# Kernel tuning notes

Measured on AMD Instinct MI355X. Metric: run time of the kernel, lower is better.

## Reference

```python
import jax, jax.numpy as jnp
import numpy as np

NUM_GROUPS = 8
NUM_HEADS = 4
EPS = 1e-5


def group_norm(x, w, b):
    # x: [B, C, H, W]; normalize over (C/G, H, W) within each of G groups
    B, C, H, W = x.shape
    xg = x.reshape(B, NUM_GROUPS, C // NUM_GROUPS, H, W)
    mean = xg.mean(axis=(2, 3, 4), keepdims=True)
    var = xg.var(axis=(2, 3, 4), keepdims=True)
    xn = ((xg - mean) * jax.lax.rsqrt(var + EPS)).reshape(B, C, H, W)
    return xn * w[None, :, None, None] + b[None, :, None, None]


def setup_inputs() -> dict:
    key = jax.random.key(0)
    ks = jax.random.split(key, 7)
    B, C, H, W = 4, 256, 64, 64
    x = jax.random.normal(ks[0], (B, C, H, W), dtype=jnp.float32)
    gn_w = jax.random.normal(ks[1], (C,), dtype=jnp.float32) * 0.1 + 1.0
    gn_b = jax.random.normal(ks[2], (C,), dtype=jnp.float32) * 0.1
    qkv_w = jax.random.normal(ks[3], (3 * C, C), dtype=jnp.float32) / np.sqrt(C)
    qkv_b = jax.random.normal(ks[4], (3 * C,), dtype=jnp.float32) * 0.02
    proj_w = jax.random.normal(ks[5], (C, C), dtype=jnp.float32) / np.sqrt(C)
    proj_b = jax.random.normal(ks[6], (C,), dtype=jnp.float32) * 0.02
    return {"x": x, "gn_w": gn_w, "gn_b": gn_b, "qkv_w": qkv_w,
            "qkv_b": qkv_b, "proj_w": proj_w, "proj_b": proj_b}


def reference(x, gn_w, gn_b, qkv_w, qkv_b, proj_w, proj_b):
    B, C, H, W = x.shape
    nh = NUM_HEADS
    hd = C // nh
    scale = hd ** -0.5
    N = H * W

    h = group_norm(x, gn_w, gn_b)
    # 1x1 conv == channel matmul: [B, 3C, H, W]
    qkv = jnp.einsum('oc,bchw->bohw', qkv_w, h) + qkv_b[None, :, None, None]
    qkv = qkv.reshape(B, 3, nh, hd, N)  # matches torch .view(B,3,nh,hd,HW)
    q, k, v = qkv[:, 0], qkv[:, 1], qkv[:, 2]  # each [B, nh, hd, N]

    attn = jnp.einsum('bhdn,bhdm->bhnm', q, k) * scale  # [B, nh, N, N]
    attn = jax.nn.softmax(attn, axis=-1)
    out = jnp.einsum('bhnm,bhdm->bhdn', attn, v)  # [B, nh, hd, N]
    out = out.reshape(B, C, H, W)

    proj = jnp.einsum('oc,bchw->bohw', proj_w, out) + proj_b[None, :, None, None]
    return x + proj
```

## Files before the change

kernel.cpp:

```cpp
#include <hip/hip_runtime.h>
#include <hip/hip_bf16.h>

#define BB   4
#define CC   256
#define NN   4096
#define NH   4
#define HD   64
#define NG   8
#define GSZ  32
#define EPSV 1e-5f
#define SCALE_L2E 0.18033688f

typedef __bf16 bf16x8 __attribute__((ext_vector_type(8)));
typedef float  f32x4  __attribute__((ext_vector_type(4)));

#define MFMA16(a, b, c)  __builtin_amdgcn_mfma_f32_16x16x32_bf16((a), (b), (c), 0, 0, 0)

#if __has_builtin(__builtin_amdgcn_exp2f)
#define EXP2F __builtin_amdgcn_exp2f
#else
#define EXP2F exp2f
#endif

__device__ inline unsigned short f2bf(float f) {
    unsigned int u = __float_as_uint(f);
    u += 0x7fffu + ((u >> 16) & 1u);
    return (unsigned short)(u >> 16);
}

__device__ __forceinline__ bf16x8 pk8(const f32x4& p0, const f32x4& p1) {
    alignas(16) unsigned int u[4];
    u[0] = __builtin_amdgcn_perm(__float_as_uint(p0[1]), __float_as_uint(p0[0]), 0x07060302u);
    u[1] = __builtin_amdgcn_perm(__float_as_uint(p0[3]), __float_as_uint(p0[2]), 0x07060302u);
    u[2] = __builtin_amdgcn_perm(__float_as_uint(p1[1]), __float_as_uint(p1[0]), 0x07060302u);
    u[3] = __builtin_amdgcn_perm(__float_as_uint(p1[3]), __float_as_uint(p1[2]), 0x07060302u);
    return *reinterpret_cast<bf16x8*>(u);
}

__device__ __forceinline__ void async_ld16(void* lds, const void* g) {
    __builtin_amdgcn_global_load_lds(
        (const __attribute__((address_space(1))) unsigned int*)g,
        (__attribute__((address_space(3))) unsigned int*)lds, 16, 0, 0);
}

__global__ void k_prep(const float* __restrict__ x, float* __restrict__ stats,
                       const float* __restrict__ wq, const float* __restrict__ wp,
                       unsigned short* __restrict__ oq, unsigned short* __restrict__ op) {
    int blk = blockIdx.x;
    int t = threadIdx.x;
    if (blk >= 256) {
        int i = (blk - 256) * 256 + t;
        if (i < 3 * CC * CC) oq[i] = f2bf(wq[i]);
        if (i < CC * CC)     op[i] = f2bf(wp[i]);
        return;
    }
    int b = blk >> 6, g = (blk >> 3) & 7, s = blk & 7;
    const float* p = x + ((size_t)(b * CC + g * GSZ)) * NN + s * 16384;
    float s0 = 0.f, s1 = 0.f;
    #pragma unroll
    for (int i = 0; i < 64; ++i) { float v = p[i * 256 + t]; s0 += v; s1 += v * v; }
    #pragma unroll
    for (int m = 1; m <= 32; m <<= 1) { s0 += __shfl_xor(s0, m); s1 += __shfl_xor(s1, m); }
    __shared__ float ls[8];
    int w = t >> 6;
    if ((t & 63) == 0) { ls[w * 2] = s0; ls[w * 2 + 1] = s1; }
    __syncthreads();
    if (t == 0) {
        float a0 = ls[0] + ls[2] + ls[4] + ls[6];
        float a1 = ls[1] + ls[3] + ls[5] + ls[7];
        atomicAdd(&stats[(b * NG + g) * 2 + 0], a0);
        atomicAdd(&stats[(b * NG + g) * 2 + 1], a1);
    }
}

__global__ void k_gnapply(const float* __restrict__ x, const float* __restrict__ gw,
                          const float* __restrict__ gb, const float* __restrict__ stats,
                          unsigned short* __restrict__ ht) {
    int b = blockIdx.z, ct = blockIdx.y, nt = blockIdx.x;
    int c0 = ct * 32, n0 = nt * 64;
    int t = threadIdx.x;
    __shared__ float tile[32][65];
    const float* xp = x + ((size_t)(b * CC + c0)) * NN + n0;
    int cl = t >> 6, nl = t & 63;
    #pragma unroll
    for (int p = 0; p < 8; ++p)
        tile[p * 4 + cl][nl] = xp[(size_t)(p * 4 + cl) * NN + nl];
    float sum = stats[(b * NG + ct) * 2 + 0];
    float ssq = stats[(b * NG + ct) * 2 + 1];
    float mean = sum * (1.0f / 131072.0f);
    float var  = ssq * (1.0f / 131072.0f) - mean * mean;
    float inv  = rsqrtf(var + EPSV);
    __syncthreads();
    int nw = t >> 2, ci = (t & 3) * 8;
    alignas(16) unsigned short o8[8];
    #pragma unroll
    for (int j = 0; j < 8; ++j) {
        int c = c0 + ci + j;
        float v = (tile[ci + j][nw] - mean) * inv * gw[c] + gb[c];
        o8[j] = f2bf(v);
    }
    *reinterpret_cast<uint4*>(ht + ((size_t)(b * NN + n0 + nw)) * CC + c0 + ci) =
        *reinterpret_cast<const uint4*>(o8);
}

__global__ void __launch_bounds__(256)
k_qkv(const unsigned short* __restrict__ ht, const unsigned short* __restrict__ wq,
      const float* __restrict__ qb,
      unsigned short* __restrict__ qt, unsigned short* __restrict__ kt,
      unsigned short* __restrict__ vt) {
    int bx = blockIdx.x, by = blockIdx.y;
    int t = threadIdx.x, wave = t >> 6, lane = t & 63;
    int l15 = lane & 15, quad = lane >> 4;
    int wm = wave >> 1, wn = wave & 1;

    __shared__ alignas(16) unsigned char smem[33792];

    const char* Ag = (const char*)wq + (size_t)by * 65536;
    const char* Bg = (const char*)ht + (size_t)bx * 65536;
    int row0 = t >> 2, slot = t & 3;
    size_t a0 = (size_t)row0 * 512 + slot * 16;
    size_t a1 = a0 + 64 * 512;
    unsigned int dst0 = wave * 1024;

    auto stage = [&](int buf, int kk) {
        size_t ko = (size_t)kk * 64;
        unsigned char* Ab = smem + buf * 8192;
        unsigned char* Bb = smem + 16384 + buf * 8192;
        async_ld16(Ab + dst0,        Ag + a0 + ko);
        async_ld16(Ab + 4096 + dst0, Ag + a1 + ko);
        async_ld16(Bb + dst0,        Bg + a0 + ko);
        async_ld16(Bb + 4096 + dst0, Bg + a1 + ko);
    };

    f32x4 acc[4][4];
    #pragma unroll
    for (int i = 0; i < 4; ++i)
        #pragma unroll
        for (int j = 0; j < 4; ++j) acc[i][j] = (f32x4){0.f, 0.f, 0.f, 0.f};

    stage(0, 0);
    __syncthreads();

    for (int kk = 0; kk < 8; ++kk) {
        int cur = kk & 1;
        if (kk < 7) stage(cur ^ 1, kk + 1);
        bf16x8 af[4], bf[4];
        #pragma unroll
        for (int f = 0; f < 4; ++f) {
            af[f] = *reinterpret_cast<const bf16x8*>(smem + cur * 8192 + (wm * 64 + f * 16 + l15) * 64 + quad * 16);
            bf[f] = *reinterpret_cast<const bf16x8*>(smem + 16384 + cur * 8192 + (wn * 64 + f * 16 + l15) * 64 + quad * 16);
        }
        #pragma unroll
        for (int fm = 0; fm < 4; ++fm)
            #pragma unroll
            for (int fn = 0; fn < 4; ++fn)
                acc[fm][fn] = MFMA16(af[fm], bf[fn], acc[fm][fn]);
        __syncthreads();
    }

    int s = by >> 1;
    int nn0 = bx * 128;
    int b = nn0 >> 12, nbase = nn0 & 4095;
    if (s < 2) {
        #pragma unroll
        for (int fm = 0; fm < 4; ++fm) {
            int o = by * 128 + wm * 64 + fm * 16 + quad * 4;
            int h = (o >> 6) & 3, d0 = o & 63;
            float bias[4];
            #pragma unroll
            for (int r = 0; r < 4; ++r) bias[r] = qb[o + r];
            #pragma unroll
            for (int fn = 0; fn < 4; ++fn) {
                int n = nbase + wn * 64 + fn * 16 + l15;
                alignas(8) unsigned short o4[4];
                if (s == 0) {
                    #pragma unroll
                    for (int r = 0; r < 4; ++r) o4[r] = f2bf((acc[fm][fn][r] + bias[r]) * SCALE_L2E);
                    *reinterpret_cast<uint2*>(qt + (((size_t)(b * NH + h) * NN) + n) * HD + d0) =
                        *reinterpret_cast<const uint2*>(o4);
                } else {
                    #pragma unroll
                    for (int r = 0; r < 4; ++r) o4[r] = f2bf(acc[fm][fn][r] + bias[r]);
                    *reinterpret_cast<uint2*>(kt + (((size_t)(b * NH + h) * NN) + n) * HD + d0) =
                        *reinterpret_cast<const uint2*>(o4);
                }
            }
        }
    } else {
        unsigned short* vtile = (unsigned short*)smem;
        #pragma unroll
        for (int fm = 0; fm < 4; ++fm) {
            int o  = by * 128 + wm * 64 + fm * 16 + quad * 4;
            int ol = wm * 64 + fm * 16 + quad * 4;
            float bias[4];
            #pragma unroll
            for (int r = 0; r < 4; ++r) bias[r] = qb[o + r];
            #pragma unroll
            for (int fn = 0; fn < 4; ++fn) {
                int nl = wn * 64 + fn * 16 + l15;
                #pragma unroll
                for (int r = 0; r < 4; ++r)
                    vtile[(ol + r) * 132 + nl] = f2bf(acc[fm][fn][r] + bias[r]);
            }
        }
        __syncthreads();
        int hbase = (by - 4) * 2;
        #pragma unroll
        for (int pass = 0; pass < 8; ++pass) {
            int row  = pass * 16 + (t >> 4);
            int col0 = (t & 15) * 8;
            int nb = (col0 & ~31) | ((col0 & 16) >> 1) | ((col0 & 8) >> 1);
            const unsigned short* src = vtile + row * 132 + nb;
            uint2 lo = *reinterpret_cast<const uint2*>(src);
            uint2 hi = *reinterpret_cast<const uint2*>(src + 16);
            uint4 o4 = make_uint4(lo.x, lo.y, hi.x, hi.y);
            int h = hbase + (row >> 6), d = row & 63;
            *reinterpret_cast<uint4*>(vt + ((size_t)(b * NH + h) * HD + d) * NN + nbase + col0) = o4;
        }
    }
}

__global__ void __launch_bounds__(256, 4)
k_attn(const unsigned short* __restrict__ qt, const unsigned short* __restrict__ kt,
       const unsigned short* __restrict__ vt,
       unsigned short* __restrict__ op0, unsigned short* __restrict__ op1,
       float* __restrict__ lip) {
    int bh = blockIdx.y;
    int split = blockIdx.z;
    int t = threadIdx.x, wave = t >> 6, lane = t & 63;
    int l15 = lane & 15, quad = lane >> 4;
    int qbase = blockIdx.x * 128 + wave * 32;
    int kbase = split * 2048;
    const unsigned short* qp = qt + (size_t)bh * NN * HD;
    const unsigned short* kp = kt + (size_t)bh * NN * HD;
    const unsigned short* vp = vt + (size_t)bh * HD * NN;

    __shared__ alignas(16) unsigned char kbuf[2][8192];
    __shared__ alignas(16) unsigned char vbuf[2][8192];

    int lr8 = lane >> 3, lc8 = lane & 7;
    int swz = lc8 ^ lr8;
    const char* ksrc = (const char*)kp + (size_t)(kbase + wave * 16 + lr8) * 128 + swz * 16;
    const char* vsrc = (const char*)vp + (size_t)(wave * 16 + lr8) * 8192 + (size_t)kbase * 2 + swz * 16;
    unsigned int dstw = wave * 2048;

    auto stage = [&](int buf) {
        async_ld16(kbuf[buf] + dstw,        ksrc);
        async_ld16(kbuf[buf] + dstw + 1024, ksrc + 1024);
        ksrc += 8192;
        async_ld16(vbuf[buf] + dstw,        vsrc);
        async_ld16(vbuf[buf] + dstw + 1024, vsrc + 8 * 8192);
        vsrc += 128;
    };

    bf16x8 qaA0 = *reinterpret_cast<const bf16x8*>(qp + (size_t)(qbase + l15) * HD + quad * 8);
    bf16x8 qaA1 = *reinterpret_cast<const bf16x8*>(qp + (size_t)(qbase + l15) * HD + 32 + quad * 8);
    bf16x8 qaB0 = *reinterpret_cast<const bf16x8*>(qp + (size_t)(qbase + 16 + l15) * HD + quad * 8);
    bf16x8 qaB1 = *reinterpret_cast<const bf16x8*>(qp + (size_t)(qbase + 16 + l15) * HD + 32 + quad * 8);

    const f32x4 Z4 = (f32x4){0.f, 0.f, 0.f, 0.f};
    bf16x8 vone;
    #pragma unroll
    for (int i = 0; i < 8; ++i) vone[i] = (__bf16)1.0f;

    f32x4 OA[4], OB[4];
    #pragma unroll
    for (int i = 0; i < 4; ++i) { OA[i] = Z4; OB[i] = Z4; }
    f32x4 liAA = Z4, liBB = Z4;

    int sx = l15 & 7;

    auto compute = [&](const unsigned char* kb, const unsigned char* vbb) {
        f32x4 sA0[2], sA1[2], sB0[2], sB1[2];
        #pragma unroll
        for (int s = 0; s < 2; ++s) {
            int r0 = (s * 32 + l15) * 128;
            bf16x8 k00 = *reinterpret_cast<const bf16x8*>(kb + r0 + ((quad ^ sx) * 16));
            bf16x8 k01 = *reinterpret_cast<const bf16x8*>(kb + r0 + (((quad + 4) ^ sx) * 16));
            bf16x8 k10 = *reinterpret_cast<const bf16x8*>(kb + r0 + 2048 + ((quad ^ sx) * 16));
            bf16x8 k11 = *reinterpret_cast<const bf16x8*>(kb + r0 + 2048 + (((quad + 4) ^ sx) * 16));
            sA0[s] = MFMA16(k00, qaA0, Z4);  sA0[s] = MFMA16(k01, qaA1, sA0[s]);
            sA1[s] = MFMA16(k10, qaA0, Z4);  sA1[s] = MFMA16(k11, qaA1, sA1[s]);
            sB0[s] = MFMA16(k00, qaB0, Z4);  sB0[s] = MFMA16(k01, qaB1, sB0[s]);
            sB1[s] = MFMA16(k10, qaB0, Z4);  sB1[s] = MFMA16(k11, qaB1, sB1[s]);
        }
        #pragma unroll
        for (int s = 0; s < 2; ++s) {
            f32x4 pA0, pA1, pB0, pB1;
            #pragma unroll
            for (int r = 0; r < 4; ++r) {
                pA0[r] = EXP2F(sA0[s][r]);  pA1[r] = EXP2F(sA1[s][r]);
                pB0[r] = EXP2F(sB0[s][r]);  pB1[r] = EXP2F(sB1[s][r]);
            }
            bf16x8 fA = pk8(pA0, pA1);
            bf16x8 fB = pk8(pB0, pB1);

            liAA = MFMA16(fA, vone, liAA);
            liBB = MFMA16(fB, vone, liBB);

            #pragma unroll
            for (int dc = 0; dc < 4; ++dc) {
                const unsigned char* vrow = vbb + (dc * 16 + l15) * 128;
                bf16x8 vv = *reinterpret_cast<const bf16x8*>(vrow + (((s * 4 + quad) ^ sx) * 16));
                OA[dc] = MFMA16(fA, vv, OA[dc]);
                OB[dc] = MFMA16(fB, vv, OB[dc]);
            }
        }
    };

    stage(0);
    __syncthreads();

    for (int p = 0; p < 16; ++p) {
        stage(1);
        compute(kbuf[0], vbuf[0]);
        __syncthreads();
        if (p < 15) stage(0);
        compute(kbuf[1], vbuf[1]);
        __syncthreads();
    }

    unsigned short* op = split ? op1 : op0;
    int b = bh >> 2, h = bh & 3;
    #pragma unroll
    for (int dc = 0; dc < 4; ++dc) {
        #pragma unroll
        for (int r = 0; r < 4; ++r) {
            int qA = qbase + quad * 4 + r;
            op[((size_t)(b * NN) + qA) * CC + h * HD + dc * 16 + l15]      = f2bf(OA[dc][r]);
            op[((size_t)(b * NN) + qA + 16) * CC + h * HD + dc * 16 + l15] = f2bf(OB[dc][r]);
        }
    }
    float* lp = lip + (size_t)split * (16 * NN) + (size_t)bh * NN + qbase;
    if (l15 == 0) {
        #pragma unroll
        for (int r = 0; r < 4; ++r) {
            lp[quad * 4 + r]      = liAA[r];
            lp[16 + quad * 4 + r] = liBB[r];
        }
    }
}

__global__ void __launch_bounds__(256)
k_comb(unsigned short* ao, const unsigned short* __restrict__ p1, const float* __restrict__ lip) {
    int g = blockIdx.x * 256 + threadIdx.x;
    int d8 = g & 7;
    int h  = (g >> 3) & 3;
    int n  = (g >> 5) & 4095;
    int b  = g >> 17;
    int bh = b * 4 + h;
    float li0 = lip[(size_t)bh * NN + n];
    float li1 = lip[(size_t)16 * NN + (size_t)bh * NN + n];
    float inv = 1.0f / (li0 + li1);
    size_t idx = ((size_t)(b * NN) + n) * CC + h * HD + d8 * 8;
    uint4 u0 = *reinterpret_cast<const uint4*>(ao + idx);
    uint4 u1 = *reinterpret_cast<const uint4*>(p1 + idx);
    const unsigned short* a0 = reinterpret_cast<const unsigned short*>(&u0);
    const unsigned short* a1 = reinterpret_cast<const unsigned short*>(&u1);
    alignas(16) unsigned short o8[8];
    #pragma unroll
    for (int i = 0; i < 8; ++i) {
        float f0 = __uint_as_float((unsigned)a0[i] << 16);
        float f1 = __uint_as_float((unsigned)a1[i] << 16);
        o8[i] = f2bf((f0 + f1) * inv);
    }
    *reinterpret_cast<uint4*>(ao + idx) = *reinterpret_cast<const uint4*>(o8);
}

__global__ void __launch_bounds__(256)
k_proj(const unsigned short* __restrict__ ao, const unsigned short* __restrict__ wp,
       const float* __restrict__ pb, const float* __restrict__ x,
       float* __restrict__ out) {
    int bx = blockIdx.x, by = blockIdx.y;
    int t = threadIdx.x, wave = t >> 6, lane = t & 63;
    int l15 = lane & 15, quad = lane >> 4;
    int wm = wave >> 1, wn = wave & 1;

    __shared__ alignas(16) unsigned char At[2][4096];
    __shared__ alignas(16) unsigned char Bt[2][4096];

    const char* Ag = (const char*)wp + (size_t)by * 32768;
    const char* Bg = (const char*)ao + (size_t)bx * 32768;
    int row0 = t >> 2, slot = t & 3;
    size_t a0 = (size_t)row0 * 512 + slot * 16;
    unsigned int dst0 = wave * 1024;

    auto stage = [&](int buf, int kk) {
        size_t ko = (size_t)kk * 64;
        async_ld16(At[buf] + dst0, Ag + a0 + ko);
        async_ld16(Bt[buf] + dst0, Bg + a0 + ko);
    };

    f32x4 acc[2][2];
    #pragma unroll
    for (int i = 0; i < 2; ++i)
        #pragma unroll
        for (int j = 0; j < 2; ++j) acc[i][j] = (f32x4){0.f, 0.f, 0.f, 0.f};

    stage(0, 0);
    __syncthreads();

    for (int kk = 0; kk < 8; ++kk) {
        int cur = kk & 1;
        if (kk < 7) stage(cur ^ 1, kk + 1);
        bf16x8 af[2], bf[2];
        #pragma unroll
        for (int f = 0; f < 2; ++f) {
            af[f] = *reinterpret_cast<const bf16x8*>(At[cur] + (wm * 32 + f * 16 + l15) * 64 + quad * 16);
            bf[f] = *reinterpret_cast<const bf16x8*>(Bt[cur] + (wn * 32 + f * 16 + l15) * 64 + quad * 16);
        }
        #pragma unroll
        for (int fm = 0; fm < 2; ++fm)
            #pragma unroll
            for (int fn = 0; fn < 2; ++fn)
                acc[fm][fn] = MFMA16(af[fm], bf[fn], acc[fm][fn]);
        __syncthreads();
    }

    int nn0 = bx * 64;
    int b = nn0 >> 12, nbase = nn0 & 4095;
    #pragma unroll
    for (int fm = 0; fm < 2; ++fm) {
        int o = by * 64 + wm * 32 + fm * 16 + quad * 4;
        float bias[4];
        #pragma unroll
        for (int r = 0; r < 4; ++r) bias[r] = pb[o + r];
        #pragma unroll
        for (int fn = 0; fn < 2; ++fn) {
            int n = nbase + wn * 32 + fn * 16 + l15;
            #pragma unroll
            for (int r = 0; r < 4; ++r) {
                size_t idx = ((size_t)(b * CC + o + r)) * NN + n;
                out[idx] = acc[fm][fn][r] + bias[r] + x[idx];
            }
        }
    }
}

extern "C" void kernel_launch(void* const* d_in, const int* in_sizes, int n_in,
                              void* d_out, int out_size, void* d_ws, size_t ws_size,
                              hipStream_t stream) {
    const float* x     = (const float*)d_in[0];
    const float* gw    = (const float*)d_in[1];
    const float* gb    = (const float*)d_in[2];
    const float* qkvw  = (const float*)d_in[3];
    const float* qkvb  = (const float*)d_in[4];
    const float* projw = (const float*)d_in[5];
    const float* projb = (const float*)d_in[6];
    float* out = (float*)d_out;

    char* w = (char*)d_ws;
    size_t off = 0;
    unsigned short* ht = (unsigned short*)(w + off); off += (size_t)BB * NN * CC * 2;
    unsigned short* qt = (unsigned short*)(w + off); off += (size_t)BB * NH * NN * HD * 2;
    unsigned short* kt = (unsigned short*)(w + off); off += (size_t)BB * NH * NN * HD * 2;
    unsigned short* vt = (unsigned short*)(w + off); off += (size_t)BB * NH * HD * NN * 2;
    unsigned short* ao = (unsigned short*)(w + off); off += (size_t)BB * NN * CC * 2;
    unsigned short* wqb = (unsigned short*)(w + off); off += (size_t)3 * CC * CC * 2;
    unsigned short* wpb = (unsigned short*)(w + off); off += (size_t)CC * CC * 2;
    float* stats = (float*)(w + off); off += BB * NG * 2 * sizeof(float);
    float* lip   = (float*)(w + off); off += (size_t)2 * 16 * NN * sizeof(float);

    hipMemsetAsync(stats, 0, BB * NG * 2 * sizeof(float), stream);
    k_prep<<<1024, 256, 0, stream>>>(x, stats, qkvw, projw, wqb, wpb);
    k_gnapply<<<dim3(NN / 64, CC / 32, BB), 256, 0, stream>>>(x, gw, gb, stats, ht);
    k_qkv<<<dim3(BB * NN / 128, 6), 256, 0, stream>>>(ht, wqb, qkvb, qt, kt, vt);
    k_attn<<<dim3(NN / 128, BB * NH, 2), 256, 0, stream>>>(qt, kt, vt, ao, ht, lip);
    k_comb<<<2048, 256, 0, stream>>>(ao, ht, lip);
    k_proj<<<dim3(BB * NN / 64, CC / 64), 256, 0, stream>>>(ao, wpb, projb, x, out);
}
```

Measured before the change: 188.7 us.

## Split attention keys four ways and raise wave priority around MFMA blocks

Splits the key dimension of the attention kernel into four chunks instead of two. This doubles the grid (32x16x4 blocks) so more CUs are busy, and each block runs half as many iterations. The partial outputs and row sums go to extra workspace buffers and are merged in the combine kernel. It also wraps the MFMA sections in s_setprio so matrix work from different waves interleaves with the exp work. The cost is more partial-output traffic to write and read back in the combine step, plus a larger workspace.

```diff
diff --git a/kernel.cpp b/kernel.cpp
--- a/kernel.cpp
+++ b/kernel.cpp
@@ -224,13 +224,14 @@
 k_attn(const unsigned short* __restrict__ qt, const unsigned short* __restrict__ kt,
        const unsigned short* __restrict__ vt,
        unsigned short* __restrict__ op0, unsigned short* __restrict__ op1,
+       unsigned short* __restrict__ op2, unsigned short* __restrict__ op3,
        float* __restrict__ lip) {
     int bh = blockIdx.y;
     int split = blockIdx.z;
     int t = threadIdx.x, wave = t >> 6, lane = t & 63;
     int l15 = lane & 15, quad = lane >> 4;
     int qbase = blockIdx.x * 128 + wave * 32;
-    int kbase = split * 2048;
+    int kbase = split * 1024;
     const unsigned short* qp = qt + (size_t)bh * NN * HD;
     const unsigned short* kp = kt + (size_t)bh * NN * HD;
     const unsigned short* vp = vt + (size_t)bh * HD * NN;
@@ -272,6 +273,7 @@
 
     auto compute = [&](const unsigned char* kb, const unsigned char* vbb) {
         f32x4 sA0[2], sA1[2], sB0[2], sB1[2];
+        __builtin_amdgcn_s_setprio(1);
         #pragma unroll
         for (int s = 0; s < 2; ++s) {
             int r0 = (s * 32 + l15) * 128;
@@ -284,6 +286,7 @@
             sB0[s] = MFMA16(k00, qaB0, Z4);  sB0[s] = MFMA16(k01, qaB1, sB0[s]);
             sB1[s] = MFMA16(k10, qaB0, Z4);  sB1[s] = MFMA16(k11, qaB1, sB1[s]);
         }
+        __builtin_amdgcn_s_setprio(0);
         #pragma unroll
         for (int s = 0; s < 2; ++s) {
             f32x4 pA0, pA1, pB0, pB1;
@@ -295,6 +298,7 @@
             bf16x8 fA = pk8(pA0, pA1);
             bf16x8 fB = pk8(pB0, pB1);
 
+            __builtin_amdgcn_s_setprio(1);
             liAA = MFMA16(fA, vone, liAA);
             liBB = MFMA16(fB, vone, liBB);
 
@@ -305,22 +309,23 @@
                 OA[dc] = MFMA16(fA, vv, OA[dc]);
                 OB[dc] = MFMA16(fB, vv, OB[dc]);
             }
+            __builtin_amdgcn_s_setprio(0);
         }
     };
 
     stage(0);
     __syncthreads();
 
-    for (int p = 0; p < 16; ++p) {
+    for (int p = 0; p < 8; ++p) {
         stage(1);
         compute(kbuf[0], vbuf[0]);
         __syncthreads();
-        if (p < 15) stage(0);
+        if (p < 7) stage(0);
         compute(kbuf[1], vbuf[1]);
         __syncthreads();
     }
 
-    unsigned short* op = split ? op1 : op0;
+    unsigned short* op = (split == 0) ? op0 : (split == 1) ? op1 : (split == 2) ? op2 : op3;
     int b = bh >> 2, h = bh & 3;
     #pragma unroll
     for (int dc = 0; dc < 4; ++dc) {
@@ -342,27 +347,36 @@
 }
 
 __global__ void __launch_bounds__(256)
-k_comb(unsigned short* ao, const unsigned short* __restrict__ p1, const float* __restrict__ lip) {
+k_comb(unsigned short* ao, const unsigned short* __restrict__ p1,
+       const unsigned short* __restrict__ p2, const unsigned short* __restrict__ p3,
+       const float* __restrict__ lip) {
     int g = blockIdx.x * 256 + threadIdx.x;
     int d8 = g & 7;
     int h  = (g >> 3) & 3;
     int n  = (g >> 5) & 4095;
     int b  = g >> 17;
     int bh = b * 4 + h;
-    float li0 = lip[(size_t)bh * NN + n];
-    float li1 = lip[(size_t)16 * NN + (size_t)bh * NN + n];
-    float inv = 1.0f / (li0 + li1);
+    size_t lbase = (size_t)bh * NN + n;
+    float li = lip[lbase] + lip[lbase + (size_t)16 * NN]
+             + lip[lbase + (size_t)32 * NN] + lip[lbase + (size_t)48 * NN];
+    float inv = 1.0f / li;
     size_t idx = ((size_t)(b * NN) + n) * CC + h * HD + d8 * 8;
     uint4 u0 = *reinterpret_cast<const uint4*>(ao + idx);
     uint4 u1 = *reinterpret_cast<const uint4*>(p1 + idx);
+    uint4 u2 = *reinterpret_cast<const uint4*>(p2 + idx);
+    uint4 u3 = *reinterpret_cast<const uint4*>(p3 + idx);
     const unsigned short* a0 = reinterpret_cast<const unsigned short*>(&u0);
     const unsigned short* a1 = reinterpret_cast<const unsigned short*>(&u1);
+    const unsigned short* a2 = reinterpret_cast<const unsigned short*>(&u2);
+    const unsigned short* a3 = reinterpret_cast<const unsigned short*>(&u3);
     alignas(16) unsigned short o8[8];
     #pragma unroll
     for (int i = 0; i < 8; ++i) {
         float f0 = __uint_as_float((unsigned)a0[i] << 16);
         float f1 = __uint_as_float((unsigned)a1[i] << 16);
-        o8[i] = f2bf((f0 + f1) * inv);
+        float f2 = __uint_as_float((unsigned)a2[i] << 16);
+        float f3 = __uint_as_float((unsigned)a3[i] << 16);
+        o8[i] = f2bf(((f0 + f1) + (f2 + f3)) * inv);
     }
     *reinterpret_cast<uint4*>(ao + idx) = *reinterpret_cast<const uint4*>(o8);
 }
@@ -456,16 +470,18 @@
     unsigned short* kt = (unsigned short*)(w + off); off += (size_t)BB * NH * NN * HD * 2;
     unsigned short* vt = (unsigned short*)(w + off); off += (size_t)BB * NH * HD * NN * 2;
     unsigned short* ao = (unsigned short*)(w + off); off += (size_t)BB * NN * CC * 2;
+    unsigned short* p2 = (unsigned short*)(w + off); off += (size_t)BB * NN * CC * 2;
+    unsigned short* p3 = (unsigned short*)(w + off); off += (size_t)BB * NN * CC * 2;
     unsigned short* wqb = (unsigned short*)(w + off); off += (size_t)3 * CC * CC * 2;
     unsigned short* wpb = (unsigned short*)(w + off); off += (size_t)CC * CC * 2;
     float* stats = (float*)(w + off); off += BB * NG * 2 * sizeof(float);
-    float* lip   = (float*)(w + off); off += (size_t)2 * 16 * NN * sizeof(float);
+    float* lip   = (float*)(w + off); off += (size_t)4 * 16 * NN * sizeof(float);
 
     hipMemsetAsync(stats, 0, BB * NG * 2 * sizeof(float), stream);
     k_prep<<<1024, 256, 0, stream>>>(x, stats, qkvw, projw, wqb, wpb);
     k_gnapply<<<dim3(NN / 64, CC / 32, BB), 256, 0, stream>>>(x, gw, gb, stats, ht);
     k_qkv<<<dim3(BB * NN / 128, 6), 256, 0, stream>>>(ht, wqb, qkvb, qt, kt, vt);
-    k_attn<<<dim3(NN / 128, BB * NH, 2), 256, 0, stream>>>(qt, kt, vt, ao, ht, lip);
-    k_comb<<<2048, 256, 0, stream>>>(ao, ht, lip);
+    k_attn<<<dim3(NN / 128, BB * NH, 4), 256, 0, stream>>>(qt, kt, vt, ao, ht, p2, p3, lip);
+    k_comb<<<2048, 256, 0, stream>>>(ao, ht, p2, p3, lip);
     k_proj<<<dim3(BB * NN / 64, CC / 64), 256, 0, stream>>>(ao, wpb, projb, x, out);
 }
```

Result: no change. 187.4 us (-0.7%).

## Fuse split-attention combine into projection GEMM and deepen QKV GEMM prefetch

Applied to the files above, without the earlier changes.

The separate k_comb kernel, which merged the two attention split partial outputs and normalized them by the summed row sums, is removed. That merge now happens inside k_proj as it loads the B tile, with registers prefetched two k-steps ahead and manual vmcnt/lgkmcnt waits. The QKV GEMM loop switches to two tiles in flight with explicit wait counts and raw barriers instead of __syncthreads. The attention kernel raises wave priority around its MFMA sections. The aim is to save a kernel launch and a full read-modify-write of the attention output, at the cost of redundant combine work: each of the four by-blocks in k_proj recomputes it.

```diff
diff --git a/kernel.cpp b/kernel.cpp
--- a/kernel.cpp
+++ b/kernel.cpp
@@ -21,6 +21,11 @@
 #else
 #define EXP2F exp2f
 #endif
+
+#define WAITV(n)  asm volatile("s_waitcnt vmcnt(" #n ")" ::: "memory")
+#define WAITL0    asm volatile("s_waitcnt lgkmcnt(0)" ::: "memory")
+#define SBAR      __builtin_amdgcn_s_barrier()
+#define SCHED0    __builtin_amdgcn_sched_barrier(0)
 
 __device__ inline unsigned short f2bf(float f) {
     unsigned int u = __float_as_uint(f);
@@ -139,11 +144,14 @@
         for (int j = 0; j < 4; ++j) acc[i][j] = (f32x4){0.f, 0.f, 0.f, 0.f};
 
     stage(0, 0);
-    __syncthreads();
+    stage(1, 1);
 
     for (int kk = 0; kk < 8; ++kk) {
+        if (kk < 7) { WAITV(4); } else { WAITV(0); }
+        SCHED0;
+        SBAR;
+        SCHED0;
         int cur = kk & 1;
-        if (kk < 7) stage(cur ^ 1, kk + 1);
         bf16x8 af[4], bf[4];
         #pragma unroll
         for (int f = 0; f < 4; ++f) {
@@ -155,7 +163,11 @@
             #pragma unroll
             for (int fn = 0; fn < 4; ++fn)
                 acc[fm][fn] = MFMA16(af[fm], bf[fn], acc[fm][fn]);
-        __syncthreads();
+        WAITL0;
+        SCHED0;
+        SBAR;
+        SCHED0;
+        if (kk < 6) stage(cur, kk + 2);
     }
 
     int s = by >> 1;
@@ -272,6 +284,7 @@
 
     auto compute = [&](const unsigned char* kb, const unsigned char* vbb) {
         f32x4 sA0[2], sA1[2], sB0[2], sB1[2];
+        __builtin_amdgcn_s_setprio(1);
         #pragma unroll
         for (int s = 0; s < 2; ++s) {
             int r0 = (s * 32 + l15) * 128;
@@ -284,6 +297,7 @@
             sB0[s] = MFMA16(k00, qaB0, Z4);  sB0[s] = MFMA16(k01, qaB1, sB0[s]);
             sB1[s] = MFMA16(k10, qaB0, Z4);  sB1[s] = MFMA16(k11, qaB1, sB1[s]);
         }
+        __builtin_amdgcn_s_setprio(0);
         #pragma unroll
         for (int s = 0; s < 2; ++s) {
             f32x4 pA0, pA1, pB0, pB1;
@@ -295,6 +309,7 @@
             bf16x8 fA = pk8(pA0, pA1);
             bf16x8 fB = pk8(pB0, pB1);
 
+            __builtin_amdgcn_s_setprio(1);
             liAA = MFMA16(fA, vone, liAA);
             liBB = MFMA16(fB, vone, liBB);
 
@@ -305,6 +320,7 @@
                 OA[dc] = MFMA16(fA, vv, OA[dc]);
                 OB[dc] = MFMA16(fB, vv, OB[dc]);
             }
+            __builtin_amdgcn_s_setprio(0);
         }
     };
 
@@ -342,35 +358,10 @@
 }
 
 __global__ void __launch_bounds__(256)
-k_comb(unsigned short* ao, const unsigned short* __restrict__ p1, const float* __restrict__ lip) {
-    int g = blockIdx.x * 256 + threadIdx.x;
-    int d8 = g & 7;
-    int h  = (g >> 3) & 3;
-    int n  = (g >> 5) & 4095;
-    int b  = g >> 17;
-    int bh = b * 4 + h;
-    float li0 = lip[(size_t)bh * NN + n];
-    float li1 = lip[(size_t)16 * NN + (size_t)bh * NN + n];
-    float inv = 1.0f / (li0 + li1);
-    size_t idx = ((size_t)(b * NN) + n) * CC + h * HD + d8 * 8;
-    uint4 u0 = *reinterpret_cast<const uint4*>(ao + idx);
-    uint4 u1 = *reinterpret_cast<const uint4*>(p1 + idx);
-    const unsigned short* a0 = reinterpret_cast<const unsigned short*>(&u0);
-    const unsigned short* a1 = reinterpret_cast<const unsigned short*>(&u1);
-    alignas(16) unsigned short o8[8];
-    #pragma unroll
-    for (int i = 0; i < 8; ++i) {
-        float f0 = __uint_as_float((unsigned)a0[i] << 16);
-        float f1 = __uint_as_float((unsigned)a1[i] << 16);
-        o8[i] = f2bf((f0 + f1) * inv);
-    }
-    *reinterpret_cast<uint4*>(ao + idx) = *reinterpret_cast<const uint4*>(o8);
-}
-
-__global__ void __launch_bounds__(256)
-k_proj(const unsigned short* __restrict__ ao, const unsigned short* __restrict__ wp,
-       const float* __restrict__ pb, const float* __restrict__ x,
-       float* __restrict__ out) {
+k_proj(const unsigned short* __restrict__ ao, const unsigned short* __restrict__ p1,
+       const float* __restrict__ lip,
+       const unsigned short* __restrict__ wp, const float* __restrict__ pb,
+       const float* __restrict__ x, float* __restrict__ out) {
     int bx = blockIdx.x, by = blockIdx.y;
     int t = threadIdx.x, wave = t >> 6, lane = t & 63;
     int l15 = lane & 15, quad = lane >> 4;
@@ -380,16 +371,41 @@
     __shared__ alignas(16) unsigned char Bt[2][4096];
 
     const char* Ag = (const char*)wp + (size_t)by * 32768;
-    const char* Bg = (const char*)ao + (size_t)bx * 32768;
     int row0 = t >> 2, slot = t & 3;
     size_t a0 = (size_t)row0 * 512 + slot * 16;
     unsigned int dst0 = wave * 1024;
 
-    auto stage = [&](int buf, int kk) {
-        size_t ko = (size_t)kk * 64;
-        async_ld16(At[buf] + dst0, Ag + a0 + ko);
-        async_ld16(Bt[buf] + dst0, Bg + a0 + ko);
+    int gtok = bx * 64 + row0;
+    int b = gtok >> 12, n = gtok & 4095;
+    size_t obase = ((size_t)(b * NN) + n) * CC + slot * 8;
+    float inv[4];
+    #pragma unroll
+    for (int h = 0; h < 4; ++h) {
+        size_t lb = (size_t)(b * 4 + h) * NN + n;
+        inv[h] = 1.0f / (lip[lb] + lip[lb + (size_t)16 * NN]);
+    }
+
+    auto stageA = [&](int buf, int kk) {
+        async_ld16(At[buf] + dst0, Ag + a0 + (size_t)kk * 64);
     };
+    uint4 eu0, eu1, ou0, ou1;
+    auto loadB = [&](uint4& r0, uint4& r1, int kk) {
+        r0 = *reinterpret_cast<const uint4*>(ao + obase + kk * 32);
+        r1 = *reinterpret_cast<const uint4*>(p1 + obase + kk * 32);
+    };
+    auto writeB = [&](int buf, const uint4& r0, const uint4& r1, float iv) {
+        const unsigned short* q0 = reinterpret_cast<const unsigned short*>(&r0);
+        const unsigned short* q1 = reinterpret_cast<const unsigned short*>(&r1);
+        alignas(16) unsigned short o8[8];
+        #pragma unroll
+        for (int i = 0; i < 8; ++i) {
+            float f0 = __uint_as_float((unsigned)q0[i] << 16);
+            float f1 = __uint_as_float((unsigned)q1[i] << 16);
+            o8[i] = f2bf((f0 + f1) * iv);
+        }
+        *reinterpret_cast<uint4*>(Bt[buf] + row0 * 64 + slot * 16) =
+            *reinterpret_cast<const uint4*>(o8);
+    };
 
     f32x4 acc[2][2];
     #pragma unroll
@@ -397,28 +413,62 @@
         #pragma unroll
         for (int j = 0; j < 2; ++j) acc[i][j] = (f32x4){0.f, 0.f, 0.f, 0.f};
 
-    stage(0, 0);
-    __syncthreads();
-
-    for (int kk = 0; kk < 8; ++kk) {
-        int cur = kk & 1;
-        if (kk < 7) stage(cur ^ 1, kk + 1);
-        bf16x8 af[2], bf[2];
-        #pragma unroll
-        for (int f = 0; f < 2; ++f) {
-            af[f] = *reinterpret_cast<const bf16x8*>(At[cur] + (wm * 32 + f * 16 + l15) * 64 + quad * 16);
-            bf[f] = *reinterpret_cast<const bf16x8*>(Bt[cur] + (wn * 32 + f * 16 + l15) * 64 + quad * 16);
-        }
-        #pragma unroll
-        for (int fm = 0; fm < 2; ++fm)
-            #pragma unroll
-            for (int fn = 0; fn < 2; ++fn)
-                acc[fm][fn] = MFMA16(af[fm], bf[fn], acc[fm][fn]);
-        __syncthreads();
+    loadB(eu0, eu1, 0);
+    stageA(0, 0);
+    loadB(ou0, ou1, 1);
+
+    #pragma unroll
+    for (int k2 = 0; k2 < 4; ++k2) {
+        {
+            const int kk = 2 * k2;
+            WAITV(2);
+            SCHED0;
+            writeB(0, eu0, eu1, inv[kk >> 1]);
+            WAITL0;
+            SCHED0;
+            SBAR;
+            SCHED0;
+            if (kk < 7) stageA(1, kk + 1);
+            if (kk < 6) loadB(eu0, eu1, kk + 2);
+            bf16x8 af[2], bf[2];
+            #pragma unroll
+            for (int f = 0; f < 2; ++f) {
+                af[f] = *reinterpret_cast<const bf16x8*>(At[0] + (wm * 32 + f * 16 + l15) * 64 + quad * 16);
+                bf[f] = *reinterpret_cast<const bf16x8*>(Bt[0] + (wn * 32 + f * 16 + l15) * 64 + quad * 16);
+            }
+            #pragma unroll
+            for (int fm = 0; fm < 2; ++fm)
+                #pragma unroll
+                for (int fn = 0; fn < 2; ++fn)
+                    acc[fm][fn] = MFMA16(af[fm], bf[fn], acc[fm][fn]);
+        }
+        {
+            const int kk = 2 * k2 + 1;
+            if (kk < 7) { WAITV(2); } else { WAITV(0); }
+            SCHED0;
+            writeB(1, ou0, ou1, inv[kk >> 1]);
+            WAITL0;
+            SCHED0;
+            SBAR;
+            SCHED0;
+            if (kk < 7) stageA(0, kk + 1);
+            if (kk < 6) loadB(ou0, ou1, kk + 2);
+            bf16x8 af[2], bf[2];
+            #pragma unroll
+            for (int f = 0; f < 2; ++f) {
+                af[f] = *reinterpret_cast<const bf16x8*>(At[1] + (wm * 32 + f * 16 + l15) * 64 + quad * 16);
+                bf[f] = *reinterpret_cast<const bf16x8*>(Bt[1] + (wn * 32 + f * 16 + l15) * 64 + quad * 16);
+            }
+            #pragma unroll
+            for (int fm = 0; fm < 2; ++fm)
+                #pragma unroll
+                for (int fn = 0; fn < 2; ++fn)
+                    acc[fm][fn] = MFMA16(af[fm], bf[fn], acc[fm][fn]);
+        }
     }
 
     int nn0 = bx * 64;
-    int b = nn0 >> 12, nbase = nn0 & 4095;
+    int bb = nn0 >> 12, nbase = nn0 & 4095;
     #pragma unroll
     for (int fm = 0; fm < 2; ++fm) {
         int o = by * 64 + wm * 32 + fm * 16 + quad * 4;
@@ -427,10 +477,10 @@
         for (int r = 0; r < 4; ++r) bias[r] = pb[o + r];
         #pragma unroll
         for (int fn = 0; fn < 2; ++fn) {
-            int n = nbase + wn * 32 + fn * 16 + l15;
+            int nc = nbase + wn * 32 + fn * 16 + l15;
             #pragma unroll
             for (int r = 0; r < 4; ++r) {
-                size_t idx = ((size_t)(b * CC + o + r)) * NN + n;
+                size_t idx = ((size_t)(bb * CC + o + r)) * NN + nc;
                 out[idx] = acc[fm][fn][r] + bias[r] + x[idx];
             }
         }
@@ -466,6 +516,5 @@
     k_gnapply<<<dim3(NN / 64, CC / 32, BB), 256, 0, stream>>>(x, gw, gb, stats, ht);
     k_qkv<<<dim3(BB * NN / 128, 6), 256, 0, stream>>>(ht, wqb, qkvb, qt, kt, vt);
     k_attn<<<dim3(NN / 128, BB * NH, 2), 256, 0, stream>>>(qt, kt, vt, ao, ht, lip);
-    k_comb<<<2048, 256, 0, stream>>>(ao, ht, lip);
-    k_proj<<<dim3(BB * NN / 64, CC / 64), 256, 0, stream>>>(ao, wpb, projb, x, out);
-}
+    k_proj<<<dim3(BB * NN / 64, CC / 64), 256, 0, stream>>>(ao, ht, lip, wpb, projb, x, out);
+}
```

New measurement: 186.0 us. No clear change (-1.4%).
